# Performance work log

Measured on AMD Instinct MI355X. Metric: run time of the kernel, lower is better.

Reference implementation:

```python
import jax, jax.numpy as jnp
import numpy as np

N_NODES = 50000
N_EDGES = 600000
C = 128
T = 2          # layer index t
NU = 1         # DRew nu parameter
EPS = 0.0      # GIN eps


def mlp(x, W1, b1, W2, b2):
    # instantiate_mlp with final_activation=False, batch_norm=False:
    # Linear -> ReLU -> Linear
    return jax.nn.relu(x @ W1 + b1) @ W2 + b2


def setup_inputs() -> dict:
    key = jax.random.key(0)
    ks = jax.random.split(key, 16)
    node_embeddings = jax.random.normal(ks[0], (T + 1, N_NODES, C), dtype=jnp.float32)
    edge_index = jax.random.randint(ks[1], (2, N_EDGES), 0, N_NODES, dtype=jnp.int32)
    edge_weights = jax.random.randint(ks[2], (N_EDGES,), 1, T + 2, dtype=jnp.int32)  # hops 1..3
    s = 1.0 / np.sqrt(C)
    def lin(k):
        kw, kb = jax.random.split(k)
        return (jax.random.uniform(kw, (C, C), jnp.float32, -s, s),
                jax.random.uniform(kb, (C,), jnp.float32, -s, s))
    loop_W1, loop_b1 = lin(ks[3]); loop_W2, loop_b2 = lin(ks[4])
    rel_W1, rel_b1 = lin(ks[5]); rel_W2, rel_b2 = lin(ks[6])
    # T higher-hop MLPs (k = 2 .. T+1), stacked along axis 0
    hh1 = [lin(k) for k in jax.random.split(ks[7], T)]
    hh2 = [lin(k) for k in jax.random.split(ks[8], T)]
    hh_W1 = jnp.stack([w for w, _ in hh1]); hh_b1 = jnp.stack([b for _, b in hh1])
    hh_W2 = jnp.stack([w for w, _ in hh2]); hh_b2 = jnp.stack([b for _, b in hh2])
    hop_coef = jax.random.normal(ks[9], (T + 1,), dtype=jnp.float32)
    return dict(t=T, node_embeddings=node_embeddings, edge_index=edge_index,
                edge_weights=edge_weights,
                loop_W1=loop_W1, loop_b1=loop_b1, loop_W2=loop_W2, loop_b2=loop_b2,
                rel_W1=rel_W1, rel_b1=rel_b1, rel_W2=rel_W2, rel_b2=rel_b2,
                hh_W1=hh_W1, hh_b1=hh_b1, hh_W2=hh_W2, hh_b2=hh_b2,
                hop_coef=hop_coef)


def reference(t, node_embeddings, edge_index, edge_weights,
              loop_W1, loop_b1, loop_W2, loop_b2,
              rel_W1, rel_b1, rel_W2, rel_b2,
              hh_W1, hh_b1, hh_W2, hh_b2, hop_coef):
    x_t = node_embeddings[t]                       # [N, C]
    n = x_t.shape[0]
    row, col = edge_index[0], edge_index[1]        # sparse A: out[row] += X[col]
    dt = x_t.dtype

    hops = []
    # hop 1: relational MLP on current-layer embeddings
    h1 = mlp(x_t, rel_W1, rel_b1, rel_W2, rel_b2)
    m1 = (edge_weights == 1).astype(dt)[:, None]
    hops.append(jax.ops.segment_sum(h1[col] * m1, row, num_segments=n))
    # hops k = 2 .. t+1: per-hop MLP on delayed embeddings (DRew)
    for k in range(2, t + 2):
        delay = max(0, k - NU)
        hk = mlp(node_embeddings[t - delay],
                 hh_W1[k - 2], hh_b1[k - 2], hh_W2[k - 2], hh_b2[k - 2])
        mk = (edge_weights == k).astype(dt)[:, None]
        hops.append(jax.ops.segment_sum(hk[col] * mk, row, num_segments=n))

    by_hop = jnp.stack(hops)                       # [t+1, N, C]
    self_term = mlp((1.0 + EPS) * x_t, loop_W1, loop_b1, loop_W2, loop_b2)
    return self_term + jnp.einsum('k,knc->nc', hop_coef, by_hop)
```

## Files before the change

kernel.cpp:

```cpp
#include <hip/hip_runtime.h>

#define N_NODES 50000
#define N_EDGES 600000
#define C 128
#define STRIPS 3125
#define N_TASKS 3

typedef __bf16 bf16;
typedef __attribute__((ext_vector_type(8))) __bf16 bf16x8;
typedef __attribute__((ext_vector_type(4))) __bf16 bf16x4;
typedef __attribute__((ext_vector_type(2))) __bf16 bf16x2;
typedef __attribute__((ext_vector_type(4))) float f32x4;
typedef __attribute__((ext_vector_type(2))) float f32x2;

struct PtrsV { const void* p[8]; };

__device__ __forceinline__ int bf16_wild(unsigned short w) {
    int exp = (w >> 7) & 0xFF;
    int mant = w & 0x7F;
    if (exp == 0xFF) return 1;
    if (exp >= 133) return 1;
    if (exp == 0) return mant != 0 ? 1 : 0;
    if (exp <= 114) return 1;
    return 0;
}

__global__ void __launch_bounds__(64) detect_kernel(
    const unsigned short* __restrict__ emb,
    const unsigned short* __restrict__ w,
    const unsigned short* __restrict__ b,
    const unsigned short* __restrict__ hc,
    int* __restrict__ flags)
{
    int lane = threadIdx.x;
    int ce = 0, cw = 0, cb = 0, ch = 0;
    for (int j = 0; j < 4; ++j) {
        ce += bf16_wild(emb[lane * 4 + j]);
        cw += bf16_wild(w[lane * 4 + j]);
    }
    for (int j = 0; j < 2; ++j) cb += bf16_wild(b[lane * 2 + j]);
    if (lane < 3) ch = bf16_wild(hc[lane]);
    for (int off = 32; off > 0; off >>= 1) {
        ce += __shfl_down(ce, off);
        cw += __shfl_down(cw, off);
        cb += __shfl_down(cb, off);
        ch += __shfl_down(ch, off);
    }
    if (lane == 0) {
        int wf = (cw >= 16) ? 1 : 0;
        flags[0] = (ce >= 16) ? 1 : 0;
        flags[1] = wf;
        flags[2] = (cb >= 8) ? 1 : 0;
        flags[3] = (ch > 0) ? 1 : wf;
    }
}

__global__ void __launch_bounds__(256) pack_kernel(
    PtrsV wmats, PtrsV bvecs, const void* hc_raw,
    const int* __restrict__ flags,
    bf16* __restrict__ pw, float* __restrict__ cbias, float* __restrict__ ccoef)
{
    int tid = blockIdx.x * 256 + threadIdx.x;
    int wf = flags[1], bfl = flags[2], hf = flags[3];
    if (tid < 8 * 16384) {
        int m    = tid >> 14;
        int r    = tid & 16383;
        int j    = r & 7;
        int lane = (r >> 3) & 63;
        int n0   = (r >> 9) & 7;
        int kk   = r >> 12;
        int k = kk * 32 + (lane >> 4) * 8 + j;
        int n = n0 * 16 + (lane & 15);
        int idx = k * C + n + ((m == 4 || m == 5) ? 16384 : 0);
        float v = wf ? ((const float*)wmats.p[m])[idx]
                     : (float)((const bf16*)wmats.p[m])[idx];
        pw[tid] = (bf16)v;
    } else if (tid < 8 * 16384 + 1024) {
        int j = tid - 8 * 16384;
        int m = j >> 7, n = j & 127;
        int idx = n + ((m == 4 || m == 5) ? 128 : 0);
        float v = bfl ? ((const float*)bvecs.p[m])[idx]
                      : (float)((const bf16*)bvecs.p[m])[idx];
        cbias[j] = v;
    } else if (tid < 8 * 16384 + 1024 + 3) {
        int i = tid - (8 * 16384 + 1024);
        float v = hf ? ((const float*)hc_raw)[i]
                     : (float)((const bf16*)hc_raw)[i];
        ccoef[i] = v;
    }
}

__device__ __forceinline__ void run_mlp(
    const bf16x8 af[4], const bf16* __restrict__ w1, const bf16* __restrict__ w2,
    const float* __restrict__ b1, const float* __restrict__ b2,
    float oscale, bf16 (*sh)[136], int lrow, int lquad)
{
    #pragma unroll
    for (int n0 = 0; n0 < 8; ++n0) {
        const bf16x8* bp = (const bf16x8*)w1 + n0 * 64 + (lquad * 16 + lrow);
        bf16x8 bv0 = bp[0];
        bf16x8 bv1 = bp[512];
        bf16x8 bv2 = bp[1024];
        bf16x8 bv3 = bp[1536];
        f32x4 a4 = {0.f, 0.f, 0.f, 0.f};
        a4 = __builtin_amdgcn_mfma_f32_16x16x32_bf16(af[0], bv0, a4, 0, 0, 0);
        a4 = __builtin_amdgcn_mfma_f32_16x16x32_bf16(af[1], bv1, a4, 0, 0, 0);
        a4 = __builtin_amdgcn_mfma_f32_16x16x32_bf16(af[2], bv2, a4, 0, 0, 0);
        a4 = __builtin_amdgcn_mfma_f32_16x16x32_bf16(af[3], bv3, a4, 0, 0, 0);
        int n = n0 * 16 + lrow;
        float bias = b1[n];
        #pragma unroll
        for (int r = 0; r < 4; ++r) {
            float v = a4[r] + bias;
            v = v > 0.f ? v : 0.f;
            sh[lquad * 4 + r][n] = (bf16)v;
        }
    }
    bf16x8 ah[4];
    #pragma unroll
    for (int kk = 0; kk < 4; ++kk)
        ah[kk] = *(const bf16x8*)(&sh[lrow][kk * 32 + lquad * 8]);
    #pragma unroll
    for (int n0 = 0; n0 < 8; ++n0) {
        const bf16x8* bp = (const bf16x8*)w2 + n0 * 64 + (lquad * 16 + lrow);
        bf16x8 bv0 = bp[0];
        bf16x8 bv1 = bp[512];
        bf16x8 bv2 = bp[1024];
        bf16x8 bv3 = bp[1536];
        f32x4 a4 = {0.f, 0.f, 0.f, 0.f};
        a4 = __builtin_amdgcn_mfma_f32_16x16x32_bf16(ah[0], bv0, a4, 0, 0, 0);
        a4 = __builtin_amdgcn_mfma_f32_16x16x32_bf16(ah[1], bv1, a4, 0, 0, 0);
        a4 = __builtin_amdgcn_mfma_f32_16x16x32_bf16(ah[2], bv2, a4, 0, 0, 0);
        a4 = __builtin_amdgcn_mfma_f32_16x16x32_bf16(ah[3], bv3, a4, 0, 0, 0);
        int n = n0 * 16 + lrow;
        float bias = b2[n];
        #pragma unroll
        for (int r = 0; r < 4; ++r)
            sh[lquad * 4 + r][n] = (bf16)((a4[r] + bias) * oscale);
    }
}

__device__ __forceinline__ void store_strip(
    const bf16 (*sh)[136], bf16* __restrict__ dst, int lane)
{
    int row = lane >> 2;
    int cs  = (lane & 3) * 32;
    #pragma unroll
    for (int i = 0; i < 4; ++i) {
        bf16x8 v = *(const bf16x8*)(&sh[row][cs + i * 8]);
        *(bf16x8*)(dst + (size_t)row * C + cs + i * 8) = v;
    }
}

__global__ __launch_bounds__(256, 4) void mlp_kernel(
    const void* __restrict__ emb_raw,
    const bf16* __restrict__ pw,
    const float* __restrict__ cbias,
    const float* __restrict__ ccoef,
    const int* __restrict__ flags,
    bf16* __restrict__ h,
    bf16* __restrict__ hs)
{
    __shared__ bf16 sH[4][16][136];
    const int tid  = threadIdx.x;
    const int wave = tid >> 6, lane = tid & 63;
    const int wid  = blockIdx.x * 4 + wave;
    if (wid >= N_TASKS * STRIPS) return;
    const int task  = wid / STRIPS;
    const int strip = wid - task * STRIPS;
    const int node0 = strip * 16;
    const int lrow = lane & 15, lquad = lane >> 4;
    bf16 (*sh)[136] = sH[wave];

    const size_t xbase = (size_t)(2 - task) * N_NODES * C
                       + (size_t)(node0 + lrow) * C + lquad * 8;
    bf16x8 af[4];
    if (flags[0]) {
        const float* xf = (const float*)emb_raw + xbase;
        #pragma unroll
        for (int kk = 0; kk < 4; ++kk) {
            f32x4 u0 = *(const f32x4*)(xf + kk * 32);
            f32x4 u1 = *(const f32x4*)(xf + kk * 32 + 4);
            bf16x8 v;
            v[0] = (bf16)u0[0]; v[1] = (bf16)u0[1]; v[2] = (bf16)u0[2]; v[3] = (bf16)u0[3];
            v[4] = (bf16)u1[0]; v[5] = (bf16)u1[1]; v[6] = (bf16)u1[2]; v[7] = (bf16)u1[3];
            af[kk] = v;
        }
    } else {
        const bf16* xb = (const bf16*)emb_raw + xbase;
        #pragma unroll
        for (int kk = 0; kk < 4; ++kk)
            af[kk] = *(const bf16x8*)(xb + kk * 32);
    }

    if (task == 0) {
        run_mlp(af, pw, pw + 16384, cbias, cbias + 128, ccoef[0], sh, lrow, lquad);
        store_strip(sh, h + (size_t)node0 * C, lane);
        run_mlp(af, pw + 6 * 16384, pw + 7 * 16384, cbias + 6 * 128, cbias + 7 * 128,
                1.0f, sh, lrow, lquad);
        store_strip(sh, hs + (size_t)node0 * C, lane);
    } else if (task == 1) {
        run_mlp(af, pw + 2 * 16384, pw + 3 * 16384, cbias + 2 * 128, cbias + 3 * 128,
                ccoef[1], sh, lrow, lquad);
        store_strip(sh, h + (size_t)N_NODES * C + (size_t)node0 * C, lane);
    } else {
        run_mlp(af, pw + 4 * 16384, pw + 5 * 16384, cbias + 4 * 128, cbias + 5 * 128,
                ccoef[2], sh, lrow, lquad);
        store_strip(sh, h + (size_t)2 * N_NODES * C + (size_t)node0 * C, lane);
    }
}

__global__ void __launch_bounds__(256) hist_kernel(
    const int* __restrict__ erow, int* __restrict__ deg)
{
    int e = blockIdx.x * 256 + threadIdx.x;
    if (e >= N_EDGES) return;
    atomicAdd(&deg[erow[e]], 1);
}

__device__ __forceinline__ int wave_incl_scan(int v, int lane) {
    int x = v;
    #pragma unroll
    for (int d = 1; d < 64; d <<= 1) {
        int t = __shfl_up(x, d);
        if (lane >= d) x += t;
    }
    return x;
}

__global__ void __launch_bounds__(256) scanA_kernel(
    const int* __restrict__ deg, int* __restrict__ offsets, int* __restrict__ btot)
{
    __shared__ int swave[4];
    int b = blockIdx.x, tid = threadIdx.x;
    int i = b * 256 + tid;
    int lane = tid & 63, wv = tid >> 6;
    int v = (i < N_NODES) ? deg[i] : 0;
    int x = wave_incl_scan(v, lane);
    if (lane == 63) swave[wv] = x;
    __syncthreads();
    int w0 = swave[0], w1 = swave[1], w2 = swave[2], w3 = swave[3];
    int wp = (wv > 0 ? w0 : 0) + (wv > 1 ? w1 : 0) + (wv > 2 ? w2 : 0);
    if (i < N_NODES) offsets[i] = wp + x - v;
    if (tid == 0) btot[b] = w0 + w1 + w2 + w3;
}

__global__ void __launch_bounds__(256) scanB_kernel(
    const int* __restrict__ btot, int* __restrict__ bbase, int nblk)
{
    __shared__ int swave[4];
    int tid = threadIdx.x;
    int lane = tid & 63, wv = tid >> 6;
    int v = (tid < nblk) ? btot[tid] : 0;
    int x = wave_incl_scan(v, lane);
    if (lane == 63) swave[wv] = x;
    __syncthreads();
    int w0 = swave[0], w1 = swave[1], w2 = swave[2], w3 = swave[3];
    int wp = (wv > 0 ? w0 : 0) + (wv > 1 ? w1 : 0) + (wv > 2 ? w2 : 0);
    if (tid < nblk) bbase[tid] = wp + x - v;
}

__global__ void __launch_bounds__(256) scanC_kernel(
    const int* __restrict__ bbase, int* __restrict__ offsets, int* __restrict__ cursor)
{
    int i = blockIdx.x * 256 + threadIdx.x;
    if (i < N_NODES) {
        int o = offsets[i] + bbase[blockIdx.x];
        offsets[i] = o;
        cursor[i] = o;
    }
    if (i == 0) offsets[N_NODES] = N_EDGES;
}

__global__ void __launch_bounds__(256) fill_kernel(
    const int* __restrict__ erow, const int* __restrict__ ecol,
    const int* __restrict__ ew,
    int* __restrict__ cursor, int* __restrict__ edata)
{
    int e = blockIdx.x * 256 + threadIdx.x;
    if (e >= N_EDGES) return;
    int dst = erow[e];
    int pos = atomicAdd(&cursor[dst], 1);
    edata[pos] = (ecol[e] << 2) | (ew[e] - 1);
}

__global__ void __launch_bounds__(256) gather_kernel(
    const int* __restrict__ offsets, const int* __restrict__ edata,
    const bf16* __restrict__ h,
    const bf16* __restrict__ hs,
    void* __restrict__ out,
    const int* __restrict__ flags)
{
    const int node = blockIdx.x * 4 + (threadIdx.x >> 6);
    if (node >= N_NODES) return;
    const int lane = threadIdx.x & 63;
    const int c = lane * 2;

    bf16x2 sv = *(const bf16x2*)(hs + (size_t)node * C + c);
    float a0 = (float)sv[0], a1 = (float)sv[1];

    const int s = offsets[node], e = offsets[node + 1];
    for (int base = s; base < e; base += 64) {
        int idx = base + lane;
        int ed_i = (idx < e) ? edata[idx] : 0;
        int cnt = e - base; if (cnt > 64) cnt = 64;
        int j = 0;
        for (; j + 4 <= cnt; j += 4) {
            int e0 = __shfl(ed_i, j);
            int e1 = __shfl(ed_i, j + 1);
            int e2 = __shfl(ed_i, j + 2);
            int e3 = __shfl(ed_i, j + 3);
            bf16x2 v0 = *(const bf16x2*)(h + (size_t)(e0 & 3) * (N_NODES * C) + (size_t)(e0 >> 2) * C + c);
            bf16x2 v1 = *(const bf16x2*)(h + (size_t)(e1 & 3) * (N_NODES * C) + (size_t)(e1 >> 2) * C + c);
            bf16x2 v2 = *(const bf16x2*)(h + (size_t)(e2 & 3) * (N_NODES * C) + (size_t)(e2 >> 2) * C + c);
            bf16x2 v3 = *(const bf16x2*)(h + (size_t)(e3 & 3) * (N_NODES * C) + (size_t)(e3 >> 2) * C + c);
            a0 += (float)v0[0] + (float)v1[0] + (float)v2[0] + (float)v3[0];
            a1 += (float)v0[1] + (float)v1[1] + (float)v2[1] + (float)v3[1];
        }
        for (; j < cnt; ++j) {
            int ed = __shfl(ed_i, j);
            bf16x2 v = *(const bf16x2*)(h + (size_t)(ed & 3) * (N_NODES * C) + (size_t)(ed >> 2) * C + c);
            a0 += (float)v[0];
            a1 += (float)v[1];
        }
    }

    if (flags[0]) {
        f32x2 o; o[0] = a0; o[1] = a1;
        *(f32x2*)((float*)out + (size_t)node * C + c) = o;
    } else {
        bf16x2 o; o[0] = (bf16)a0; o[1] = (bf16)a1;
        *(bf16x2*)((bf16*)out + (size_t)node * C + c) = o;
    }
}

extern "C" void kernel_launch(void* const* d_in, const int* in_sizes, int n_in,
                              void* d_out, int out_size, void* d_ws, size_t ws_size,
                              hipStream_t stream) {
    const void* emb = d_in[1];
    const int*  ei  = (const int*)d_in[2];
    const int*  ew  = (const int*)d_in[3];

    const size_t H_BYTES  = (size_t)3 * N_NODES * C * sizeof(bf16);
    const size_t HS_BYTES = (size_t)N_NODES * C * sizeof(bf16);
    const size_t PW_BYTES = (size_t)8 * 16384 * sizeof(bf16);
    bf16*  h      = (bf16*)d_ws;
    bf16*  hs     = (bf16*)((char*)d_ws + H_BYTES);
    bf16*  pw     = (bf16*)((char*)d_ws + H_BYTES + HS_BYTES);
    float* cbias  = (float*)((char*)d_ws + H_BYTES + HS_BYTES + PW_BYTES);
    float* ccoef  = cbias + 1024;
    int*   flags  = (int*)(ccoef + 4);
    int*   deg    = flags + 16;
    int*   cursor = deg + N_NODES;
    int*   offsets= cursor + N_NODES;
    int*   btot   = offsets + N_NODES + 8;
    int*   bbase  = btot + 256;
    int*   edata  = bbase + 256;

    PtrsV wptr;
    wptr.p[0] = d_in[8];   wptr.p[1] = d_in[10];
    wptr.p[2] = d_in[12];  wptr.p[3] = d_in[14];
    wptr.p[4] = d_in[12];  wptr.p[5] = d_in[14];
    wptr.p[6] = d_in[4];   wptr.p[7] = d_in[6];
    PtrsV bptr;
    bptr.p[0] = d_in[9];   bptr.p[1] = d_in[11];
    bptr.p[2] = d_in[13];  bptr.p[3] = d_in[15];
    bptr.p[4] = d_in[13];  bptr.p[5] = d_in[15];
    bptr.p[6] = d_in[5];   bptr.p[7] = d_in[7];

    detect_kernel<<<1, 64, 0, stream>>>(
        (const unsigned short*)emb, (const unsigned short*)d_in[8],
        (const unsigned short*)d_in[9], (const unsigned short*)d_in[16], flags);

    pack_kernel<<<517, 256, 0, stream>>>(wptr, bptr, d_in[16], flags, pw, cbias, ccoef);

    hipMemsetAsync(deg, 0, N_NODES * sizeof(int), stream);
    const int* erow = ei;
    const int* ecol = ei + N_EDGES;
    const int NBLK = (N_NODES + 255) / 256;
    hist_kernel<<<(N_EDGES + 255) / 256, 256, 0, stream>>>(erow, deg);
    scanA_kernel<<<NBLK, 256, 0, stream>>>(deg, offsets, btot);
    scanB_kernel<<<1, 256, 0, stream>>>(btot, bbase, NBLK);
    scanC_kernel<<<NBLK, 256, 0, stream>>>(bbase, offsets, cursor);
    fill_kernel<<<(N_EDGES + 255) / 256, 256, 0, stream>>>(erow, ecol, ew, cursor, edata);

    const int n_waves = N_TASKS * STRIPS;
    mlp_kernel<<<(n_waves + 3) / 4, 256, 0, stream>>>(emb, pw, cbias, ccoef, flags, h, hs);

    gather_kernel<<<(N_NODES + 3) / 4, 256, 0, stream>>>(
        offsets, edata, h, hs, d_out, flags);
}
```

Measured before the change: 294.0 us.

## Make MLP kernel persistent with register-resident weights and prefetch

The MLP kernel becomes persistent: 1024 waves each own one of four weight sets, hold W1/W2 fragments and biases in registers, and loop over strips with the next strip's input prefetched. This removes the repeated weight reloads per strip. The self-loop MLP is split into its own wave set instead of running after the hop-1 MLP in the same wave. The memset of the degree array is folded into the detect kernel, and the gather loop gains an 8-wide unrolled block. Keeping 64 bf16x8 weight fragments per lane needs many registers and caps occupancy at one block per CU, so latency hiding relies on the prefetch.

New measurement: 302.8 us. 3.0% more time.

```diff
diff --git a/kernel.cpp b/kernel.cpp
--- a/kernel.cpp
+++ b/kernel.cpp
@@ -4,7 +4,7 @@
 #define N_EDGES 600000
 #define C 128
 #define STRIPS 3125
-#define N_TASKS 3
+#define MLP_WAVES 1024
 
 typedef __bf16 bf16;
 typedef __attribute__((ext_vector_type(8))) __bf16 bf16x8;
@@ -25,33 +25,39 @@
     return 0;
 }
 
-__global__ void __launch_bounds__(64) detect_kernel(
+__global__ void __launch_bounds__(256) detect_zero_kernel(
     const unsigned short* __restrict__ emb,
     const unsigned short* __restrict__ w,
     const unsigned short* __restrict__ b,
     const unsigned short* __restrict__ hc,
-    int* __restrict__ flags)
-{
-    int lane = threadIdx.x;
-    int ce = 0, cw = 0, cb = 0, ch = 0;
-    for (int j = 0; j < 4; ++j) {
-        ce += bf16_wild(emb[lane * 4 + j]);
-        cw += bf16_wild(w[lane * 4 + j]);
-    }
-    for (int j = 0; j < 2; ++j) cb += bf16_wild(b[lane * 2 + j]);
-    if (lane < 3) ch = bf16_wild(hc[lane]);
-    for (int off = 32; off > 0; off >>= 1) {
-        ce += __shfl_down(ce, off);
-        cw += __shfl_down(cw, off);
-        cb += __shfl_down(cb, off);
-        ch += __shfl_down(ch, off);
-    }
-    if (lane == 0) {
-        int wf = (cw >= 16) ? 1 : 0;
-        flags[0] = (ce >= 16) ? 1 : 0;
-        flags[1] = wf;
-        flags[2] = (cb >= 8) ? 1 : 0;
-        flags[3] = (ch > 0) ? 1 : wf;
+    int* __restrict__ flags, int* __restrict__ deg)
+{
+    if (blockIdx.x == 0) {
+        int lane = threadIdx.x;
+        if (lane >= 64) return;
+        int ce = 0, cw = 0, cb = 0, ch = 0;
+        for (int j = 0; j < 4; ++j) {
+            ce += bf16_wild(emb[lane * 4 + j]);
+            cw += bf16_wild(w[lane * 4 + j]);
+        }
+        for (int j = 0; j < 2; ++j) cb += bf16_wild(b[lane * 2 + j]);
+        if (lane < 3) ch = bf16_wild(hc[lane]);
+        for (int off = 32; off > 0; off >>= 1) {
+            ce += __shfl_down(ce, off);
+            cw += __shfl_down(cw, off);
+            cb += __shfl_down(cb, off);
+            ch += __shfl_down(ch, off);
+        }
+        if (lane == 0) {
+            int wf = (cw >= 16) ? 1 : 0;
+            flags[0] = (ce >= 16) ? 1 : 0;
+            flags[1] = wf;
+            flags[2] = (cb >= 8) ? 1 : 0;
+            flags[3] = (ch > 0) ? 1 : wf;
+        }
+    } else {
+        int i = (blockIdx.x - 1) * 256 + threadIdx.x;
+        if (i < N_NODES) deg[i] = 0;
     }
 }
 
@@ -90,69 +96,7 @@
     }
 }
 
-__device__ __forceinline__ void run_mlp(
-    const bf16x8 af[4], const bf16* __restrict__ w1, const bf16* __restrict__ w2,
-    const float* __restrict__ b1, const float* __restrict__ b2,
-    float oscale, bf16 (*sh)[136], int lrow, int lquad)
-{
-    #pragma unroll
-    for (int n0 = 0; n0 < 8; ++n0) {
-        const bf16x8* bp = (const bf16x8*)w1 + n0 * 64 + (lquad * 16 + lrow);
-        bf16x8 bv0 = bp[0];
-        bf16x8 bv1 = bp[512];
-        bf16x8 bv2 = bp[1024];
-        bf16x8 bv3 = bp[1536];
-        f32x4 a4 = {0.f, 0.f, 0.f, 0.f};
-        a4 = __builtin_amdgcn_mfma_f32_16x16x32_bf16(af[0], bv0, a4, 0, 0, 0);
-        a4 = __builtin_amdgcn_mfma_f32_16x16x32_bf16(af[1], bv1, a4, 0, 0, 0);
-        a4 = __builtin_amdgcn_mfma_f32_16x16x32_bf16(af[2], bv2, a4, 0, 0, 0);
-        a4 = __builtin_amdgcn_mfma_f32_16x16x32_bf16(af[3], bv3, a4, 0, 0, 0);
-        int n = n0 * 16 + lrow;
-        float bias = b1[n];
-        #pragma unroll
-        for (int r = 0; r < 4; ++r) {
-            float v = a4[r] + bias;
-            v = v > 0.f ? v : 0.f;
-            sh[lquad * 4 + r][n] = (bf16)v;
-        }
-    }
-    bf16x8 ah[4];
-    #pragma unroll
-    for (int kk = 0; kk < 4; ++kk)
-        ah[kk] = *(const bf16x8*)(&sh[lrow][kk * 32 + lquad * 8]);
-    #pragma unroll
-    for (int n0 = 0; n0 < 8; ++n0) {
-        const bf16x8* bp = (const bf16x8*)w2 + n0 * 64 + (lquad * 16 + lrow);
-        bf16x8 bv0 = bp[0];
-        bf16x8 bv1 = bp[512];
-        bf16x8 bv2 = bp[1024];
-        bf16x8 bv3 = bp[1536];
-        f32x4 a4 = {0.f, 0.f, 0.f, 0.f};
-        a4 = __builtin_amdgcn_mfma_f32_16x16x32_bf16(ah[0], bv0, a4, 0, 0, 0);
-        a4 = __builtin_amdgcn_mfma_f32_16x16x32_bf16(ah[1], bv1, a4, 0, 0, 0);
-        a4 = __builtin_amdgcn_mfma_f32_16x16x32_bf16(ah[2], bv2, a4, 0, 0, 0);
-        a4 = __builtin_amdgcn_mfma_f32_16x16x32_bf16(ah[3], bv3, a4, 0, 0, 0);
-        int n = n0 * 16 + lrow;
-        float bias = b2[n];
-        #pragma unroll
-        for (int r = 0; r < 4; ++r)
-            sh[lquad * 4 + r][n] = (bf16)((a4[r] + bias) * oscale);
-    }
-}
-
-__device__ __forceinline__ void store_strip(
-    const bf16 (*sh)[136], bf16* __restrict__ dst, int lane)
-{
-    int row = lane >> 2;
-    int cs  = (lane & 3) * 32;
-    #pragma unroll
-    for (int i = 0; i < 4; ++i) {
-        bf16x8 v = *(const bf16x8*)(&sh[row][cs + i * 8]);
-        *(bf16x8*)(dst + (size_t)row * C + cs + i * 8) = v;
-    }
-}
-
-__global__ __launch_bounds__(256, 4) void mlp_kernel(
+__global__ __launch_bounds__(256, 1) void mlp_kernel(
     const void* __restrict__ emb_raw,
     const bf16* __restrict__ pw,
     const float* __restrict__ cbias,
@@ -165,48 +109,109 @@
     const int tid  = threadIdx.x;
     const int wave = tid >> 6, lane = tid & 63;
     const int wid  = blockIdx.x * 4 + wave;
-    if (wid >= N_TASKS * STRIPS) return;
-    const int task  = wid / STRIPS;
-    const int strip = wid - task * STRIPS;
-    const int node0 = strip * 16;
+    const int set  = wid & 3;
+    const int wstart = wid >> 2;
     const int lrow = lane & 15, lquad = lane >> 4;
     bf16 (*sh)[136] = sH[wave];
 
-    const size_t xbase = (size_t)(2 - task) * N_NODES * C
-                       + (size_t)(node0 + lrow) * C + lquad * 8;
-    bf16x8 af[4];
-    if (flags[0]) {
-        const float* xf = (const float*)emb_raw + xbase;
+    const int mat1_of[4]  = {0, 2, 4, 6};
+    const int layer_of[4] = {2, 1, 0, 2};
+    const int m1 = mat1_of[set];
+    const bf16x8* w1v = (const bf16x8*)(pw + (size_t)m1 * 16384);
+    const bf16x8* w2v = w1v + 2048;
+    const float* b1 = cbias + m1 * 128;
+    const float* b2 = b1 + 128;
+    const float oscale = (set == 0) ? ccoef[0] : (set == 1) ? ccoef[1]
+                       : (set == 2) ? ccoef[2] : 1.0f;
+    bf16* outp = (set == 3) ? hs : (h + (size_t)set * N_NODES * C);
+    const int emb_f32 = flags[0];
+    const size_t lbase = (size_t)layer_of[set] * N_NODES * C;
+
+    bf16x8 W1f[8][4], W2f[8][4];
+    #pragma unroll
+    for (int n0 = 0; n0 < 8; ++n0)
         #pragma unroll
         for (int kk = 0; kk < 4; ++kk) {
-            f32x4 u0 = *(const f32x4*)(xf + kk * 32);
-            f32x4 u1 = *(const f32x4*)(xf + kk * 32 + 4);
-            bf16x8 v;
-            v[0] = (bf16)u0[0]; v[1] = (bf16)u0[1]; v[2] = (bf16)u0[2]; v[3] = (bf16)u0[3];
-            v[4] = (bf16)u1[0]; v[5] = (bf16)u1[1]; v[6] = (bf16)u1[2]; v[7] = (bf16)u1[3];
-            af[kk] = v;
-        }
-    } else {
-        const bf16* xb = (const bf16*)emb_raw + xbase;
+            W1f[n0][kk] = w1v[kk * 512 + n0 * 64 + lane];
+            W2f[n0][kk] = w2v[kk * 512 + n0 * 64 + lane];
+        }
+    float b1f[8], b2f[8];
+    #pragma unroll
+    for (int n0 = 0; n0 < 8; ++n0) {
+        b1f[n0] = b1[n0 * 16 + lrow];
+        b2f[n0] = b2[n0 * 16 + lrow];
+    }
+
+    auto loadA = [&](int strip, bf16x8 af[4]) {
+        size_t xb = lbase + (size_t)(strip * 16 + lrow) * C + lquad * 8;
+        if (emb_f32) {
+            const float* xf = (const float*)emb_raw + xb;
+            #pragma unroll
+            for (int kk = 0; kk < 4; ++kk) {
+                f32x4 u0 = *(const f32x4*)(xf + kk * 32);
+                f32x4 u1 = *(const f32x4*)(xf + kk * 32 + 4);
+                bf16x8 v;
+                v[0]=(bf16)u0[0]; v[1]=(bf16)u0[1]; v[2]=(bf16)u0[2]; v[3]=(bf16)u0[3];
+                v[4]=(bf16)u1[0]; v[5]=(bf16)u1[1]; v[6]=(bf16)u1[2]; v[7]=(bf16)u1[3];
+                af[kk] = v;
+            }
+        } else {
+            const bf16* x16 = (const bf16*)emb_raw + xb;
+            #pragma unroll
+            for (int kk = 0; kk < 4; ++kk)
+                af[kk] = *(const bf16x8*)(x16 + kk * 32);
+        }
+    };
+
+    bf16x8 af[4];
+    if (wstart < STRIPS) loadA(wstart, af);
+    for (int s = wstart; s < STRIPS; s += 256) {
+        #pragma unroll
+        for (int n0 = 0; n0 < 8; ++n0) {
+            f32x4 a4 = {0.f, 0.f, 0.f, 0.f};
+            #pragma unroll
+            for (int kk = 0; kk < 4; ++kk)
+                a4 = __builtin_amdgcn_mfma_f32_16x16x32_bf16(af[kk], W1f[n0][kk], a4, 0, 0, 0);
+            float bias = b1f[n0];
+            int n = n0 * 16 + lrow;
+            #pragma unroll
+            for (int r = 0; r < 4; ++r) {
+                float v = a4[r] + bias;
+                v = v > 0.f ? v : 0.f;
+                sh[lquad * 4 + r][n] = (bf16)v;
+            }
+        }
+        bf16x8 afn[4];
+        int snext = s + 256;
+        if (snext < STRIPS) loadA(snext, afn);
+        bf16x8 ah[4];
         #pragma unroll
         for (int kk = 0; kk < 4; ++kk)
-            af[kk] = *(const bf16x8*)(xb + kk * 32);
-    }
-
-    if (task == 0) {
-        run_mlp(af, pw, pw + 16384, cbias, cbias + 128, ccoef[0], sh, lrow, lquad);
-        store_strip(sh, h + (size_t)node0 * C, lane);
-        run_mlp(af, pw + 6 * 16384, pw + 7 * 16384, cbias + 6 * 128, cbias + 7 * 128,
-                1.0f, sh, lrow, lquad);
-        store_strip(sh, hs + (size_t)node0 * C, lane);
-    } else if (task == 1) {
-        run_mlp(af, pw + 2 * 16384, pw + 3 * 16384, cbias + 2 * 128, cbias + 3 * 128,
-                ccoef[1], sh, lrow, lquad);
-        store_strip(sh, h + (size_t)N_NODES * C + (size_t)node0 * C, lane);
-    } else {
-        run_mlp(af, pw + 4 * 16384, pw + 5 * 16384, cbias + 4 * 128, cbias + 5 * 128,
-                ccoef[2], sh, lrow, lquad);
-        store_strip(sh, h + (size_t)2 * N_NODES * C + (size_t)node0 * C, lane);
+            ah[kk] = *(const bf16x8*)(&sh[lrow][kk * 32 + lquad * 8]);
+        #pragma unroll
+        for (int n0 = 0; n0 < 8; ++n0) {
+            f32x4 a4 = {0.f, 0.f, 0.f, 0.f};
+            #pragma unroll
+            for (int kk = 0; kk < 4; ++kk)
+                a4 = __builtin_amdgcn_mfma_f32_16x16x32_bf16(ah[kk], W2f[n0][kk], a4, 0, 0, 0);
+            float bias = b2f[n0];
+            int n = n0 * 16 + lrow;
+            #pragma unroll
+            for (int r = 0; r < 4; ++r)
+                sh[lquad * 4 + r][n] = (bf16)((a4[r] + bias) * oscale);
+        }
+        {
+            int row = lane >> 2;
+            int cs  = (lane & 3) * 32;
+            bf16* dst = outp + (size_t)(s * 16) * C;
+            #pragma unroll
+            for (int i = 0; i < 4; ++i) {
+                bf16x8 v = *(const bf16x8*)(&sh[row][cs + i * 8]);
+                *(bf16x8*)(dst + (size_t)row * C + cs + i * 8) = v;
+            }
+        }
+        #pragma unroll
+        for (int kk = 0; kk < 4; ++kk) af[kk] = afn[kk];
     }
 }
 
@@ -305,6 +310,18 @@
         int ed_i = (idx < e) ? edata[idx] : 0;
         int cnt = e - base; if (cnt > 64) cnt = 64;
         int j = 0;
+        for (; j + 8 <= cnt; j += 8) {
+            float t0 = 0.f, t1 = 0.f;
+            #pragma unroll
+            for (int u = 0; u < 8; ++u) {
+                int ed = __shfl(ed_i, j + u);
+                bf16x2 v = *(const bf16x2*)(h + (size_t)(ed & 3) * (N_NODES * C)
+                                              + (size_t)(ed >> 2) * C + c);
+                t0 += (float)v[0];
+                t1 += (float)v[1];
+            }
+            a0 += t0; a1 += t1;
+        }
         for (; j + 4 <= cnt; j += 4) {
             int e0 = __shfl(ed_i, j);
             int e1 = __shfl(ed_i, j + 1);
@@ -368,24 +385,24 @@
     bptr.p[4] = d_in[13];  bptr.p[5] = d_in[15];
     bptr.p[6] = d_in[5];   bptr.p[7] = d_in[7];
 
-    detect_kernel<<<1, 64, 0, stream>>>(
+    const int NBLK = (N_NODES + 255) / 256;
+
+    detect_zero_kernel<<<1 + NBLK, 256, 0, stream>>>(
         (const unsigned short*)emb, (const unsigned short*)d_in[8],
-        (const unsigned short*)d_in[9], (const unsigned short*)d_in[16], flags);
+        (const unsigned short*)d_in[9], (const unsigned short*)d_in[16],
+        flags, deg);
 
     pack_kernel<<<517, 256, 0, stream>>>(wptr, bptr, d_in[16], flags, pw, cbias, ccoef);
 
-    hipMemsetAsync(deg, 0, N_NODES * sizeof(int), stream);
     const int* erow = ei;
     const int* ecol = ei + N_EDGES;
-    const int NBLK = (N_NODES + 255) / 256;
     hist_kernel<<<(N_EDGES + 255) / 256, 256, 0, stream>>>(erow, deg);
     scanA_kernel<<<NBLK, 256, 0, stream>>>(deg, offsets, btot);
     scanB_kernel<<<1, 256, 0, stream>>>(btot, bbase, NBLK);
     scanC_kernel<<<NBLK, 256, 0, stream>>>(bbase, offsets, cursor);
     fill_kernel<<<(N_EDGES + 255) / 256, 256, 0, stream>>>(erow, ecol, ew, cursor, edata);
 
-    const int n_waves = N_TASKS * STRIPS;
-    mlp_kernel<<<(n_waves + 3) / 4, 256, 0, stream>>>(emb, pw, cbias, ccoef, flags, h, hs);
+    mlp_kernel<<<MLP_WAVES / 4, 256, 0, stream>>>(emb, pw, cbias, ccoef, flags, h, hs);
 
     gather_kernel<<<(N_NODES + 3) / 4, 256, 0, stream>>>(
         offsets, edata, h, hs, d_out, flags);
```
